# Optimization experiments

Measured on AMD Instinct MI355X. Metric: run time of the kernel, lower is better.

Reference implementation:

```python
import jax, jax.numpy as jnp
import numpy as np

B, T = 8, 256
IDIM = 80; ODIM = 80; HDIM = 256; CDIM = 64
TEMPER = 1.0; ETH = 40.0
N_ITER = HDIM // CDIM  # 4


def shift_windows(key, pad, window):
    # key: (B,T,D) -> all shifted windows (B,T,S,window), S = D + 2*pad - window + 1
    D = key.shape[-1]
    kp = jnp.pad(key, ((0, 0), (0, 0), (pad, pad)))
    S = D + 2 * pad - window + 1
    idx = jnp.arange(S)[:, None] + jnp.arange(window)[None, :]
    return kp[..., idx]


def sim_argmax(x_aug, y):
    # cosine similarity over feature dim, argmax over shift dim S
    num = jnp.einsum('btsw,btw->bts', x_aug, y)
    den = jnp.sqrt(jnp.sum(x_aug ** 2, -1)) * jnp.sqrt(jnp.sum(y ** 2, -1))[..., None] + 1e-6
    sim = num / den
    theta = jnp.argmax(sim, -1)  # (B,T)
    y_al = jnp.take_along_axis(x_aug, theta[..., None, None], 2)[..., 0, :]
    s_opt = jnp.take_along_axis(sim, theta[..., None], -1)[..., 0]
    return y_al, s_opt, theta


def reverse_shift(y_al, pad, window, theta, D):
    # place aligned window back at its original offset (inverse of shift theta)
    yp = jnp.pad(y_al, ((0, 0), (0, 0), (pad, pad)))
    S = window + 2 * pad - D + 1
    idx = jnp.arange(S)[:, None] + jnp.arange(D)[None, :]
    win = yp[..., idx]  # (B,T,S,D)
    start = 2 * pad - theta
    return jnp.take_along_axis(win, start[..., None, None], 2)[..., 0, :]


def attention(x, y, temper):
    return jax.nn.softmax(x * y / temper, axis=-1)


def seq_loss(pred, tgt, mask):
    # elementwise MSE, zeroed at padded positions (mask True)
    return jnp.where(mask, 0.0, (pred - tgt) ** 2)


def hsr(h, mask_prev, seq_mask_t):
    # topk energy masking with cross-iteration exclusivity (hidden-space regularization)
    idx = jax.lax.top_k(h ** 2, CDIM)[1]
    mask_cur = jax.nn.one_hot(idx, HDIM, dtype=h.dtype).sum(-2)
    if mask_prev is None:
        mask_new, loss_h = mask_cur, None
    else:
        inter = mask_prev * mask_cur
        lh = jnp.where(seq_mask_t[..., None], 0.0, (h - (1.0 - inter)) ** 2)
        loss_h = jnp.sum(jnp.where(inter > 0, lh, 0.0))
        h = jnp.where(mask_prev > 0, 0.0, h)
        idx = jax.lax.top_k(h ** 2, CDIM)[1]
        mask_cur = jax.nn.one_hot(idx, HDIM, dtype=h.dtype).sum(-2)
        mask_new = mask_prev + mask_cur
    return h * mask_cur, mask_new, loss_h


def conv1d_encode(z, W, b, D):
    # windowed encoder: all D+1 offsets of a width-2D window, pick max-energy offset
    zw = shift_windows(z, D, 2 * D)                 # (B,T,D+1,2D)
    h = jnp.einsum('btsw,wh->btsh', zw, W) + b      # (B,T,D+1,H)
    ind = jnp.argmax(jnp.sum(h ** 2, -1), -1)       # (B,T)
    h_sel = jnp.take_along_axis(h, ind[..., None, None], 2)[..., 0, :]
    return h_sel, ind


def conv1d_decode(h, W, b, ind, D):
    # gather length-D slice starting at the encoder's chosen offset
    ext = jnp.einsum('bth,hw->btw', h, W) + b       # (B,T,2D)
    idx = ind[..., None] + jnp.arange(D)            # (B,T,D)
    return jnp.take_along_axis(ext, idx, -1)


def _forward(x, y, We, be, Wd, bd, Wds, bds):
    seq_mask = (y == 0.0)                 # ignore_out = 0.0
    seq_mask_t = jnp.all(seq_mask, -1)    # per-timestep padding flag
    y_res, x_res = y, x
    mp_src = mp_self = None
    losses = []
    for _ in range(N_ITER):
        x_aug = shift_windows(x_res, ODIM - 1, ODIM)
        y_al, s_opt, theta = sim_argmax(x_aug, y_res)
        attn = attention(y_al, y_res, TEMPER)
        x_ele = reverse_shift(y_al * attn, ODIM - 1, ODIM, theta, IDIM)
        # self branch (conv1d)
        h_self, ind_self = conv1d_encode(x_ele, We, be, IDIM)
        h_self, mp_self, lh_self = hsr(h_self, mp_self, seq_mask_t)
        x_ele = conv1d_decode(h_self, Wds, bds, ind_self, IDIM)
        move = jnp.abs(theta - IDIM + 1)[..., None]
        ll_self = jnp.where(move > ETH, 0.0, seq_loss(x_ele, x_res, seq_mask)) / (move.astype(x.dtype) + 1.0)
        # re-align decoded x_ele to y_res
        x_aug = shift_windows(x_ele, ODIM - 1, ODIM)
        y_al, s_opt, theta = sim_argmax(x_aug, y_res)
        # src branch (conv1d)
        h_src, ind_src = conv1d_encode(y_al, We, be, IDIM)
        h_src, mp_src, lh_src = hsr(h_src, mp_src, seq_mask_t)
        y_ele = conv1d_decode(h_src, Wd, bd, ind_src, ODIM)
        move = jnp.abs(theta - ODIM + 1)[..., None]
        ll_src = jnp.where(move > ETH, 0.0, seq_loss(y_ele, y_res, seq_mask)) / (move.astype(x.dtype) + 1.0)
        loss_it = ll_src.sum() + ll_self.sum()
        if lh_src is not None:
            loss_it = loss_it + lh_src + lh_self
        losses.append(loss_it)
        y_res = jax.lax.stop_gradient(y_res - y_ele)
        x_res = jax.lax.stop_gradient(x_res - x_ele)
    return jnp.mean(jnp.stack(losses))


def setup_inputs() -> dict:
    key = jax.random.key(0)
    ks = jax.random.split(key, 8)
    return {
        'x': jax.random.normal(ks[0], (B, T, IDIM), jnp.float32),
        'y': jax.random.normal(ks[1], (B, T, ODIM), jnp.float32),
        'We': jax.random.normal(ks[2], (2 * IDIM, HDIM), jnp.float32) * 0.05,
        'be': jnp.zeros((HDIM,), jnp.float32),
        'Wd': jax.random.normal(ks[3], (HDIM, 2 * ODIM), jnp.float32) * 0.05,
        'bd': jnp.zeros((2 * ODIM,), jnp.float32),
        'Wds': jax.random.normal(ks[4], (HDIM, 2 * IDIM), jnp.float32) * 0.05,
        'bds': jnp.zeros((2 * IDIM,), jnp.float32),
    }


def reference(x, y, We, be, Wd, bd, Wds, bds):
    return _forward(x, y, We, be, Wd, bd, Wds, bds)
```

## Files before the change

kernel.cpp:

```cpp
#include <hip/hip_runtime.h>
#include <math.h>

#define NBT 2048

typedef __attribute__((ext_vector_type(8))) short short8;
typedef __attribute__((ext_vector_type(4))) float floatx4;

struct SM {
  alignas(16) float xp[240];
  alignas(16) short xhr[8][264];
  alignas(16) short xlr[8][264];
  alignas(16) unsigned long long hkey[256];
  alignas(16) float yres[80];
  alignas(16) float beL[256];
  alignas(16) float spad[240];
  alignas(16) int2  dpair[64];
  alignas(16) float energyP[4][96];
  float xres[80];
  float yal[80];
  float xele[80];
  float decsrc[80];
  float zb[80];
  float energy[96];
  float mp_self[256];
  float mp_src[256];
  float ext[160];
  unsigned char smask[80];
  int smask_t;
  float abv[4];
  int   abi[4];
  int   wcnt[4];
  float nys;
};

__device__ __forceinline__ float waveSum(float v){
  #pragma unroll
  for (int off = 32; off > 0; off >>= 1) v += __shfl_xor(v, off, 64);
  return v;
}
__device__ __forceinline__ int waveSumI(int v){
  #pragma unroll
  for (int off = 32; off > 0; off >>= 1) v += __shfl_xor(v, off, 64);
  return v;
}
__device__ __forceinline__ float waveMax(float v){
  #pragma unroll
  for (int off = 32; off > 0; off >>= 1) v = fmaxf(v, __shfl_xor(v, off, 64));
  return v;
}

__device__ __forceinline__ int blockArgMax(SM& sm, float v, int idx){
  int lane = threadIdx.x & 63, w = threadIdx.x >> 6;
  #pragma unroll
  for (int off = 32; off > 0; off >>= 1){
    float ov = __shfl_xor(v,   off, 64);
    int   oi = __shfl_xor(idx, off, 64);
    if (ov > v || (ov == v && oi < idx)){ v = ov; idx = oi; }
  }
  if (lane == 0){ sm.abv[w] = v; sm.abi[w] = idx; }
  __syncthreads();
  float bv = sm.abv[0]; int bi = sm.abi[0];
  #pragma unroll
  for (int w2 = 1; w2 < 4; w2++){
    float ov = sm.abv[w2]; int oi = sm.abi[w2];
    if (ov > bv || (ov == bv && oi < bi)){ bv = ov; bi = oi; }
  }
  __syncthreads();
  return bi;
}

__device__ __forceinline__ int rankTop64(SM& sm, unsigned long long mykey){
  int cnt = 0;
  const ulonglong2* q2 = (const ulonglong2*)sm.hkey;
  #pragma unroll 8
  for (int i2 = 0; i2 < 128; i2++){
    ulonglong2 o = q2[i2];
    cnt += (o.x > mykey) ? 1 : 0;
    cnt += (o.y > mykey) ? 1 : 0;
  }
  return (cnt < 64) ? 1 : 0;
}
__device__ __forceinline__ unsigned long long rankKey(float vsq, int j){
  return (((unsigned long long)__float_as_uint(vsq)) << 8)
       | (unsigned long long)(255 - j);
}

__device__ __forceinline__ void compactSel(SM& sm, int sel, float val){
  int tid = threadIdx.x, lane = tid & 63, w = tid >> 6;
  unsigned long long mq = __ballot(sel != 0);
  if (lane == 0) sm.wcnt[w] = __popcll(mq);
  __syncthreads();
  int base = 0;
  #pragma unroll
  for (int i = 0; i < 4; i++) base += (i < w) ? sm.wcnt[i] : 0;
  if (sel){
    unsigned long long below = (lane == 0) ? 0ull : ((~0ull) >> (64 - lane));
    int pos = base + (int)__popcll(mq & below);
    sm.dpair[pos] = make_int2(tid, __float_as_int(val));
  }
  __syncthreads();
}

__device__ __forceinline__ int simArgmax(SM& sm, const float* src, float* yal_out, int doNy){
  int tid = threadIdx.x;
  int lane = tid & 63, w = tid >> 6;
  __syncthreads();
  if (tid < 240) sm.spad[tid] = (tid >= 79 && tid < 159) ? src[tid - 79] : 0.f;
  if (doNy && w == 0){
    float yv2 = 0.f;
    for (int i = lane; i < 80; i += 64){ float yv = sm.yres[i]; yv2 = fmaf(yv, yv, yv2); }
    float ny = sqrtf(waveSum(yv2));
    if (lane == 0) sm.nys = ny;
  }
  __syncthreads();
  float nys = sm.nys;
  float bv = -INFINITY; int bi = 0;
  if (tid < 159){
    const float4* y4p = (const float4*)sm.yres;
    float num = 0.f, nx = 0.f;
    for (int w4 = 0; w4 < 20; w4++){
      float4 yy = y4p[w4];
      int wb = w4 * 4;
      float xa0 = sm.spad[tid + wb + 0];
      float xa1 = sm.spad[tid + wb + 1];
      float xa2 = sm.spad[tid + wb + 2];
      float xa3 = sm.spad[tid + wb + 3];
      num = fmaf(xa0, yy.x, num); nx = fmaf(xa0, xa0, nx);
      num = fmaf(xa1, yy.y, num); nx = fmaf(xa1, xa1, nx);
      num = fmaf(xa2, yy.z, num); nx = fmaf(xa2, xa2, nx);
      num = fmaf(xa3, yy.w, num); nx = fmaf(xa3, xa3, nx);
    }
    bv = num / (sqrtf(nx) * nys + 1e-6f);
    bi = tid;
  }
  int th = blockArgMax(sm, bv, bi);
  if (tid < 80) yal_out[tid] = sm.spad[th + tid];
  __syncthreads();
  return th;
}

template<int USE_WS>
__device__ __forceinline__ void branchCompute(
    SM& sm, const float* __restrict__ We,
    const short8* __restrict__ wsB,
    const float* __restrict__ Wdec, const float* __restrict__ bdec,
    const float* enc_in, float* mask, const float* target,
    float* dec_out, int theta, bool first, float& lossAcc)
{
  int tid = threadIdx.x;
  int lane = tid & 63, w = tid >> 6;
  int quad = lane >> 4, l15 = lane & 15;
  __syncthreads();
  {
    float v = (tid >= 80 && tid < 160) ? enc_in[tid - 80] : 0.f;
    if (tid < 240) sm.xp[tid] = v;
    unsigned bits = __float_as_uint(v);
    unsigned hi = bits >> 16;
    float hif = __uint_as_float(hi << 16);
    unsigned lo = __float_as_uint(v - hif) >> 16;
    short hs = (short)hi, ls = (short)lo;
    #pragma unroll
    for (int c = 0; c < 8; c++){
      int i = tid - c;
      if (i >= 0){ sm.xhr[c][i] = hs; sm.xlr[c][i] = ls; }
    }
  }
  __syncthreads();

  const floatx4 zero4 = {0.f, 0.f, 0.f, 0.f};
  const int ng = w;
  const int c8 = l15 & 7;
  const int hb = l15 >> 3;

  #pragma unroll 1
  for (int mh = 0; mh < 3; mh++){
    int ktlo = (mh == 0) ? 1 : 0;
    int kthi = 5 - mh;
    floatx4 acc[2][4];
    #pragma unroll
    for (int m2 = 0; m2 < 2; m2++)
      #pragma unroll
      for (int nt = 0; nt < 4; nt++) acc[m2][nt] = zero4;

    #pragma unroll 1
    for (int kt = ktlo; kt < kthi; kt++){
      short8 Ah[2], Al[2];
      #pragma unroll
      for (int m2 = 0; m2 < 2; m2++){
        int mt = mh * 2 + m2;
        int kb = quad + 2 * mt + 4 * kt + hb;
        Ah[m2] = *reinterpret_cast<const short8*>(&sm.xhr[c8][8 * kb]);
        Al[m2] = *reinterpret_cast<const short8*>(&sm.xlr[c8][8 * kb]);
      }
      #pragma unroll 2
      for (int nt = 0; nt < 4; nt++){
        short8 Bh, Bl;
        int tileIdx = kt * 16 + (ng * 4 + nt);
        if (USE_WS){
          int ti2 = (tileIdx * 64 + lane) * 2;
          Bh = wsB[ti2];
          Bl = wsB[ti2 + 1];
        } else {
          short8 bh, bl;
          int k0 = kt * 32 + quad * 8;
          int n  = (ng * 4 + nt) * 16 + l15;
          #pragma unroll
          for (int j = 0; j < 8; j++){
            float v = We[(k0 + j) * 256 + n];
            unsigned bits = __float_as_uint(v);
            unsigned hi = bits >> 16;
            float hif = __uint_as_float(hi << 16);
            unsigned lo = __float_as_uint(v - hif) >> 16;
            bh[j] = (short)hi; bl[j] = (short)lo;
          }
          Bh = bh; Bl = bl;
        }
        acc[0][nt] = __builtin_amdgcn_mfma_f32_16x16x32_bf16(Ah[0], Bh, acc[0][nt], 0, 0, 0);
        acc[0][nt] = __builtin_amdgcn_mfma_f32_16x16x32_bf16(Al[0], Bh, acc[0][nt], 0, 0, 0);
        acc[0][nt] = __builtin_amdgcn_mfma_f32_16x16x32_bf16(Ah[0], Bl, acc[0][nt], 0, 0, 0);
        acc[1][nt] = __builtin_amdgcn_mfma_f32_16x16x32_bf16(Ah[1], Bh, acc[1][nt], 0, 0, 0);
        acc[1][nt] = __builtin_amdgcn_mfma_f32_16x16x32_bf16(Al[1], Bh, acc[1][nt], 0, 0, 0);
        acc[1][nt] = __builtin_amdgcn_mfma_f32_16x16x32_bf16(Ah[1], Bl, acc[1][nt], 0, 0, 0);
      }
    }

    float bn[4];
    #pragma unroll
    for (int nt = 0; nt < 4; nt++) bn[nt] = sm.beL[(ng * 4 + nt) * 16 + l15];
    #pragma unroll
    for (int m2 = 0; m2 < 2; m2++){
      int mt = mh * 2 + m2;
      float er[4];
      #pragma unroll
      for (int r = 0; r < 4; r++){
        float s_ = 0.f;
        #pragma unroll
        for (int nt = 0; nt < 4; nt++){
          float hvv = acc[m2][nt][r] + bn[nt];
          s_ = fmaf(hvv, hvv, s_);
        }
        er[r] = s_;
      }
      #pragma unroll
      for (int x2 = 1; x2 < 16; x2 <<= 1){
        #pragma unroll
        for (int r = 0; r < 4; r++) er[r] += __shfl_xor(er[r], x2, 64);
      }
      if (l15 == 0){
        #pragma unroll
        for (int r = 0; r < 4; r++)
          sm.energyP[w][mt * 16 + quad * 4 + r] = er[r];
      }
    }
  }
  __syncthreads();
  if (tid < 96){
    float e = sm.energyP[0][tid];
    e += sm.energyP[1][tid];
    e += sm.energyP[2][tid];
    e += sm.energyP[3][tid];
    sm.energy[tid] = e;
  }
  __syncthreads();

  float bvE = (tid < 81) ? sm.energy[tid] : -INFINITY;
  int   biE = (tid < 81) ? tid : 0;
  int ind = blockArgMax(sm, bvE, biE);

  int roff = 80 - ind;
  float hv = sm.beL[tid];
  #pragma unroll 8
  for (int w2 = 0; w2 < 80; w2++){
    float xv = sm.xp[80 + w2];
    hv = fmaf(xv, We[(w2 + roff) * 256 + tid], hv);
  }

  float vsq = hv * hv;
  unsigned long long myk = rankKey(vsq, tid);
  sm.hkey[tid] = myk;
  __syncthreads();
  int sel1 = rankTop64(sm, myk);
  float mpv = mask[tid];
  if (first){
    mask[tid] = (float)sel1;
    compactSel(sm, sel1, hv);
  } else {
    int st = sm.smask_t;
    float interv = mpv * (float)sel1;
    if (interv > 0.f && !st){
      float dd = hv - (1.f - interv);
      lossAcc += dd * dd;
    }
    float h2 = (mpv > 0.f) ? 0.f : hv;
    __syncthreads();
    unsigned long long myk2 = rankKey(h2 * h2, tid);
    sm.hkey[tid] = myk2;
    __syncthreads();
    int sel2 = rankTop64(sm, myk2);
    mask[tid] = mpv + (float)sel2;
    compactSel(sm, sel2, h2);
  }

  if (tid < 160){
    float a = bdec[tid];
    #pragma unroll 8
    for (int i = 0; i < 64; i++){
      int2 p = sm.dpair[i];
      a = fmaf(__int_as_float(p.y), Wdec[p.x * 160 + tid], a);
    }
    sm.ext[tid] = a;
  }
  __syncthreads();

  float mv = fabsf((float)(theta - 79));
  bool gate = (mv > 40.0f);
  if (tid < 80){
    float dec = sm.ext[ind + tid];
    dec_out[tid] = dec;
    float diff = dec - target[tid];
    float l = (gate || sm.smask[tid]) ? 0.f : diff * diff;
    lossAcc += l / (mv + 1.0f);
  }
  __syncthreads();
}

__global__ void __launch_bounds__(64) zero_out_kernel(float* out){
  if (threadIdx.x == 0) out[0] = 0.f;
}

__global__ void __launch_bounds__(64) prep_we_kernel(
    const float* __restrict__ We, short8* __restrict__ wsB){
  int tile = blockIdx.x;
  int lane = threadIdx.x;
  int kt = tile >> 4, nt = tile & 15;
  int k0 = kt * 32 + (lane >> 4) * 8;
  int n  = nt * 16 + (lane & 15);
  short8 h, l;
  #pragma unroll
  for (int j = 0; j < 8; j++){
    float v = We[(k0 + j) * 256 + n];
    unsigned bits = __float_as_uint(v);
    unsigned hi = bits >> 16;
    float hif = __uint_as_float(hi << 16);
    unsigned lo = __float_as_uint(v - hif) >> 16;
    h[j] = (short)hi; l[j] = (short)lo;
  }
  int ti2 = (tile * 64 + lane) * 2;
  wsB[ti2]     = h;
  wsB[ti2 + 1] = l;
}

template<int USE_WS>
__global__ void __launch_bounds__(256, 4) net_kernel(
    const float* __restrict__ x,  const float* __restrict__ y,
    const float* __restrict__ We, const float* __restrict__ be,
    const float* __restrict__ Wd, const float* __restrict__ bd,
    const float* __restrict__ Wds,const float* __restrict__ bds,
    const short8* __restrict__ wsB,
    float* out)
{
  __shared__ SM sm;
  int tid = threadIdx.x;
  int lane = tid & 63, w = tid >> 6;
  int bt  = blockIdx.x;
  const float* xin = x + bt * 80;
  const float* yin = y + bt * 80;

  if (tid < 80){
    sm.xres[tid] = xin[tid];
    float yv = yin[tid];
    sm.yres[tid] = yv;
    sm.smask[tid] = (yv == 0.f) ? 1 : 0;
  }
  sm.mp_self[tid] = 0.f;
  sm.mp_src[tid]  = 0.f;
  sm.beL[tid] = be[tid];
  __syncthreads();
  if (w == 0){
    int c = 0;
    for (int i = lane; i < 80; i += 64) c += (int)sm.smask[i];
    int total = waveSumI(c);
    if (lane == 0) sm.smask_t = (total == 80) ? 1 : 0;
  }
  __syncthreads();

  float lossAcc = 0.f;

  for (int it = 0; it < 4; it++){
    bool first = (it == 0);

    int th1 = simArgmax(sm, sm.xres, sm.yal, 1);

    if (w == 0){
      float p0 = sm.yal[lane] * sm.yres[lane];
      float p1 = (lane < 16) ? sm.yal[64 + lane] * sm.yres[64 + lane] : -INFINITY;
      float mx = waveMax(fmaxf(p0, p1));
      float e0 = expf(p0 - mx);
      float e1 = (lane < 16) ? expf(p1 - mx) : 0.f;
      float ssum = waveSum(e0 + e1);
      sm.zb[lane] = sm.yal[lane] * (e0 / ssum);
      if (lane < 16) sm.zb[64 + lane] = sm.yal[64 + lane] * (e1 / ssum);
    }
    __syncthreads();

    if (tid < 80){
      int q = tid + 79 - th1;
      sm.xele[tid] = (q >= 0 && q < 80) ? sm.zb[q] : 0.f;
    }

    branchCompute<USE_WS>(sm, We, wsB, Wds, bds,
                          sm.xele, sm.mp_self, sm.xres, sm.xele, th1, first, lossAcc);

    int th2 = simArgmax(sm, sm.xele, sm.yal, 0);

    branchCompute<USE_WS>(sm, We, wsB, Wd, bd,
                          sm.yal, sm.mp_src, sm.yres, sm.decsrc, th2, first, lossAcc);

    __syncthreads();
    if (tid < 80){
      sm.xres[tid] -= sm.xele[tid];
      sm.yres[tid] -= sm.decsrc[tid];
    }
    __syncthreads();
  }

  float vsum = waveSum(lossAcc);
  if (lane == 0) sm.abv[w] = vsum;
  __syncthreads();
  if (tid == 0){
    float total = ((sm.abv[0] + sm.abv[1]) + sm.abv[2]) + sm.abv[3];
    atomicAdd(out, total * 0.25f);
  }
}

extern "C" void kernel_launch(void* const* d_in, const int* in_sizes, int n_in,
                              void* d_out, int out_size, void* d_ws, size_t ws_size,
                              hipStream_t stream) {
  const float* x   = (const float*)d_in[0];
  const float* y   = (const float*)d_in[1];
  const float* We  = (const float*)d_in[2];
  const float* be  = (const float*)d_in[3];
  const float* Wd  = (const float*)d_in[4];
  const float* bd  = (const float*)d_in[5];
  const float* Wds = (const float*)d_in[6];
  const float* bds = (const float*)d_in[7];
  float* out = (float*)d_out;

  const size_t fragCount = 80 * 64 * 2;
  const size_t fragBytes = fragCount * sizeof(short8);
  int use_ws = (ws_size >= fragBytes) ? 1 : 0;
  short8* wsB = (short8*)d_ws;

  hipLaunchKernelGGL(zero_out_kernel, dim3(1), dim3(64), 0, stream, out);
  if (use_ws){
    hipLaunchKernelGGL(prep_we_kernel, dim3(80), dim3(64), 0, stream, We, wsB);
    hipLaunchKernelGGL((net_kernel<1>), dim3(NBT), dim3(256), 0, stream,
                       x, y, We, be, Wd, bd, Wds, bds, wsB, out);
  } else {
    hipLaunchKernelGGL((net_kernel<0>), dim3(NBT), dim3(256), 0, stream,
                       x, y, We, be, Wd, bd, Wds, bds, wsB, out);
  }
}
```

Baseline: 641.5 us.

## Shrink registers and LDS to double occupancy with 32-bit top-k ranking keys

The top-k rank keys move from 64-bit packed value/index to 32-bit float bits, and ties are resolved by index comparison only within each wave's own segment. The hidden-mask arrays become bytes instead of floats, which shrinks shared memory. The MFMA encoder loop now processes one M-tile per iteration instead of two, which cuts accumulator register pressure, and launch bounds rise from 4 to 8 blocks per CU. The aim is higher occupancy and cheaper rank comparisons, at the cost of fewer independent MFMAs in flight per wave. The tie handling only covers the wave's own 64 keys, so it should be checked against the old packed-key ordering.

```diff
diff --git a/kernel.cpp b/kernel.cpp
--- a/kernel.cpp
+++ b/kernel.cpp
@@ -10,7 +10,7 @@
   alignas(16) float xp[240];
   alignas(16) short xhr[8][264];
   alignas(16) short xlr[8][264];
-  alignas(16) unsigned long long hkey[256];
+  alignas(16) unsigned hkey[256];
   alignas(16) float yres[80];
   alignas(16) float beL[256];
   alignas(16) float spad[240];
@@ -22,8 +22,8 @@
   float decsrc[80];
   float zb[80];
   float energy[96];
-  float mp_self[256];
-  float mp_src[256];
+  unsigned char mp_self[256];
+  unsigned char mp_src[256];
   float ext[160];
   unsigned char smask[80];
   int smask_t;
@@ -69,20 +69,36 @@
   return bi;
 }
 
-__device__ __forceinline__ int rankTop64(SM& sm, unsigned long long mykey){
+__device__ __forceinline__ int rankTop64(SM& sm, unsigned myb, int tid, int w){
   int cnt = 0;
-  const ulonglong2* q2 = (const ulonglong2*)sm.hkey;
-  #pragma unroll 8
-  for (int i2 = 0; i2 < 128; i2++){
-    ulonglong2 o = q2[i2];
-    cnt += (o.x > mykey) ? 1 : 0;
-    cnt += (o.y > mykey) ? 1 : 0;
+  const uint4* q4 = (const uint4*)sm.hkey;
+  int b0 = 16 * w, b1 = b0 + 16;
+  #pragma unroll 4
+  for (int i4 = 0; i4 < b0; i4++){
+    uint4 o = q4[i4];
+    cnt += (o.x >= myb) ? 1 : 0;
+    cnt += (o.y >= myb) ? 1 : 0;
+    cnt += (o.z >= myb) ? 1 : 0;
+    cnt += (o.w >= myb) ? 1 : 0;
+  }
+  #pragma unroll 4
+  for (int i4 = b0; i4 < b1; i4++){
+    uint4 o = q4[i4];
+    int i = 4 * i4;
+    cnt += ((o.x > myb) || (o.x == myb && (i    ) < tid)) ? 1 : 0;
+    cnt += ((o.y > myb) || (o.y == myb && (i + 1) < tid)) ? 1 : 0;
+    cnt += ((o.z > myb) || (o.z == myb && (i + 2) < tid)) ? 1 : 0;
+    cnt += ((o.w > myb) || (o.w == myb && (i + 3) < tid)) ? 1 : 0;
+  }
+  #pragma unroll 4
+  for (int i4 = b1; i4 < 64; i4++){
+    uint4 o = q4[i4];
+    cnt += (o.x > myb) ? 1 : 0;
+    cnt += (o.y > myb) ? 1 : 0;
+    cnt += (o.z > myb) ? 1 : 0;
+    cnt += (o.w > myb) ? 1 : 0;
   }
   return (cnt < 64) ? 1 : 0;
-}
-__device__ __forceinline__ unsigned long long rankKey(float vsq, int j){
-  return (((unsigned long long)__float_as_uint(vsq)) << 8)
-       | (unsigned long long)(255 - j);
 }
 
 __device__ __forceinline__ void compactSel(SM& sm, int sel, float val){
@@ -144,7 +160,7 @@
     SM& sm, const float* __restrict__ We,
     const short8* __restrict__ wsB,
     const float* __restrict__ Wdec, const float* __restrict__ bdec,
-    const float* enc_in, float* mask, const float* target,
+    const float* enc_in, unsigned char* mask, const float* target,
     float* dec_out, int theta, bool first, float& lossAcc)
 {
   int tid = threadIdx.x;
@@ -173,26 +189,19 @@
   const int hb = l15 >> 3;
 
   #pragma unroll 1
-  for (int mh = 0; mh < 3; mh++){
-    int ktlo = (mh == 0) ? 1 : 0;
-    int kthi = 5 - mh;
-    floatx4 acc[2][4];
+  for (int mt = 0; mt < 6; mt++){
+    const int ktlo = (mt == 0) ? 2 : ((mt <= 2) ? 1 : 0);
+    const int kthi = (mt <= 1) ? 5 : ((mt <= 3) ? 4 : 3);
+    floatx4 acc[4];
     #pragma unroll
-    for (int m2 = 0; m2 < 2; m2++)
-      #pragma unroll
-      for (int nt = 0; nt < 4; nt++) acc[m2][nt] = zero4;
+    for (int nt = 0; nt < 4; nt++) acc[nt] = zero4;
 
     #pragma unroll 1
     for (int kt = ktlo; kt < kthi; kt++){
-      short8 Ah[2], Al[2];
-      #pragma unroll
-      for (int m2 = 0; m2 < 2; m2++){
-        int mt = mh * 2 + m2;
-        int kb = quad + 2 * mt + 4 * kt + hb;
-        Ah[m2] = *reinterpret_cast<const short8*>(&sm.xhr[c8][8 * kb]);
-        Al[m2] = *reinterpret_cast<const short8*>(&sm.xlr[c8][8 * kb]);
-      }
-      #pragma unroll 2
+      int kb = quad + 2 * mt + 4 * kt + hb;
+      short8 Ah = *reinterpret_cast<const short8*>(&sm.xhr[c8][8 * kb]);
+      short8 Al = *reinterpret_cast<const short8*>(&sm.xlr[c8][8 * kb]);
+      #pragma unroll 1
       for (int nt = 0; nt < 4; nt++){
         short8 Bh, Bl;
         int tileIdx = kt * 16 + (ng * 4 + nt);
@@ -215,42 +224,35 @@
           }
           Bh = bh; Bl = bl;
         }
-        acc[0][nt] = __builtin_amdgcn_mfma_f32_16x16x32_bf16(Ah[0], Bh, acc[0][nt], 0, 0, 0);
-        acc[0][nt] = __builtin_amdgcn_mfma_f32_16x16x32_bf16(Al[0], Bh, acc[0][nt], 0, 0, 0);
-        acc[0][nt] = __builtin_amdgcn_mfma_f32_16x16x32_bf16(Ah[0], Bl, acc[0][nt], 0, 0, 0);
-        acc[1][nt] = __builtin_amdgcn_mfma_f32_16x16x32_bf16(Ah[1], Bh, acc[1][nt], 0, 0, 0);
-        acc[1][nt] = __builtin_amdgcn_mfma_f32_16x16x32_bf16(Al[1], Bh, acc[1][nt], 0, 0, 0);
-        acc[1][nt] = __builtin_amdgcn_mfma_f32_16x16x32_bf16(Ah[1], Bl, acc[1][nt], 0, 0, 0);
+        acc[nt] = __builtin_amdgcn_mfma_f32_16x16x32_bf16(Ah, Bh, acc[nt], 0, 0, 0);
+        acc[nt] = __builtin_amdgcn_mfma_f32_16x16x32_bf16(Al, Bh, acc[nt], 0, 0, 0);
+        acc[nt] = __builtin_amdgcn_mfma_f32_16x16x32_bf16(Ah, Bl, acc[nt], 0, 0, 0);
       }
     }
 
     float bn[4];
     #pragma unroll
     for (int nt = 0; nt < 4; nt++) bn[nt] = sm.beL[(ng * 4 + nt) * 16 + l15];
+    float er[4];
     #pragma unroll
-    for (int m2 = 0; m2 < 2; m2++){
-      int mt = mh * 2 + m2;
-      float er[4];
+    for (int r = 0; r < 4; r++){
+      float s_ = 0.f;
       #pragma unroll
-      for (int r = 0; r < 4; r++){
-        float s_ = 0.f;
-        #pragma unroll
-        for (int nt = 0; nt < 4; nt++){
-          float hvv = acc[m2][nt][r] + bn[nt];
-          s_ = fmaf(hvv, hvv, s_);
-        }
-        er[r] = s_;
+      for (int nt = 0; nt < 4; nt++){
+        float hvv = acc[nt][r] + bn[nt];
+        s_ = fmaf(hvv, hvv, s_);
       }
+      er[r] = s_;
+    }
+    #pragma unroll
+    for (int x2 = 1; x2 < 16; x2 <<= 1){
       #pragma unroll
-      for (int x2 = 1; x2 < 16; x2 <<= 1){
-        #pragma unroll
-        for (int r = 0; r < 4; r++) er[r] += __shfl_xor(er[r], x2, 64);
-      }
-      if (l15 == 0){
-        #pragma unroll
-        for (int r = 0; r < 4; r++)
-          sm.energyP[w][mt * 16 + quad * 4 + r] = er[r];
-      }
+      for (int r = 0; r < 4; r++) er[r] += __shfl_xor(er[r], x2, 64);
+    }
+    if (l15 == 0){
+      #pragma unroll
+      for (int r = 0; r < 4; r++)
+        sm.energyP[w][mt * 16 + quad * 4 + r] = er[r];
     }
   }
   __syncthreads();
@@ -276,28 +278,28 @@
   }
 
   float vsq = hv * hv;
-  unsigned long long myk = rankKey(vsq, tid);
-  sm.hkey[tid] = myk;
-  __syncthreads();
-  int sel1 = rankTop64(sm, myk);
-  float mpv = mask[tid];
+  unsigned myb = __float_as_uint(vsq);
+  sm.hkey[tid] = myb;
+  __syncthreads();
+  int sel1 = rankTop64(sm, myb, tid, w);
+  unsigned char mpv = mask[tid];
   if (first){
-    mask[tid] = (float)sel1;
+    mask[tid] = (unsigned char)sel1;
     compactSel(sm, sel1, hv);
   } else {
     int st = sm.smask_t;
-    float interv = mpv * (float)sel1;
+    float interv = (float)mpv * (float)sel1;
     if (interv > 0.f && !st){
       float dd = hv - (1.f - interv);
       lossAcc += dd * dd;
     }
-    float h2 = (mpv > 0.f) ? 0.f : hv;
+    float h2 = (mpv > 0) ? 0.f : hv;
     __syncthreads();
-    unsigned long long myk2 = rankKey(h2 * h2, tid);
-    sm.hkey[tid] = myk2;
+    unsigned myb2 = __float_as_uint(h2 * h2);
+    sm.hkey[tid] = myb2;
     __syncthreads();
-    int sel2 = rankTop64(sm, myk2);
-    mask[tid] = mpv + (float)sel2;
+    int sel2 = rankTop64(sm, myb2, tid, w);
+    mask[tid] = (unsigned char)(mpv + (unsigned char)sel2);
     compactSel(sm, sel2, h2);
   }
 
@@ -351,7 +353,7 @@
 }
 
 template<int USE_WS>
-__global__ void __launch_bounds__(256, 4) net_kernel(
+__global__ void __launch_bounds__(256, 8) net_kernel(
     const float* __restrict__ x,  const float* __restrict__ y,
     const float* __restrict__ We, const float* __restrict__ be,
     const float* __restrict__ Wd, const float* __restrict__ bd,
@@ -372,8 +374,8 @@
     sm.yres[tid] = yv;
     sm.smask[tid] = (yv == 0.f) ? 1 : 0;
   }
-  sm.mp_self[tid] = 0.f;
-  sm.mp_src[tid]  = 0.f;
+  sm.mp_self[tid] = 0;
+  sm.mp_src[tid]  = 0;
   sm.beL[tid] = be[tid];
   __syncthreads();
   if (w == 0){
```

New measurement: 678.7 us. 1.06x slower.
